# Kernel tuning notes

Hardware: AMD Instinct MI355X
Metric: run time of the kernel (lower is better)

The kernel has to match this reference:

```python
import jax, jax.numpy as jnp
import numpy as np

B, L, HID = 512, 128, 384
N_LABELS, N_SLOTS = 32, 128


def setup_inputs() -> dict:
    key = jax.random.key(0)
    ks = jax.random.split(key, 16)

    def g(k, shape, scale):
        return jax.random.normal(k, shape, dtype=jnp.float32) * scale

    sent_lens = jax.random.randint(ks[0], (B,), 1, L + 1)
    mask = (jnp.arange(L)[None, :] < sent_lens[:, None]).astype(jnp.float32)[..., None]
    # zero out padded token positions to mimic the ragged original
    H = g(ks[1], (B, L, HID), 1.0) * mask
    c_slot_cont = g(ks[2], (B, L, HID), 1.0) * mask
    c_inte = g(ks[3], (B, HID), 1.0)
    s = 1.0 / np.sqrt(HID)
    return {
        "H": H,
        "c_slot_cont": c_slot_cont,
        "c_inte": c_inte,
        "W0": g(ks[4], (HID, HID), s),
        "W1": g(ks[5], (HID, HID), s),
        "W2": g(ks[6], (HID, HID), s),
        "W3": g(ks[7], (HID, HID), s),
        "W4": g(ks[8], (HID, HID), s),
        "b4": g(ks[9], (HID,), s),
        "W5": g(ks[10], (HID, 1), s),
        "V_SF": g(ks[11], (HID, HID), s),
        "W_inte": g(ks[12], (HID, N_LABELS), s),
        "W_slot": g(ks[13], (2 * HID, N_SLOTS), s),
        "sent_lens": sent_lens,
        "iteration_num": 3,
    }


def reference(H, c_slot_cont, c_inte, W0, W1, W2, W3, W4, b4, W5, V_SF,
              W_inte, W_slot, sent_lens, iteration_num):
    Ld = H.shape[1]
    mask = jnp.arange(Ld)[None, :] < sent_lens[:, None]          # [B, L] bool
    maskf = mask[..., None].astype(H.dtype)                       # [B, L, 1]
    neg_inf = jnp.finfo(H.dtype).min

    def sf_fusion(x, y):
        # SF_FusionLayer (dropout off / eval); inner loop runs once since nth=2
        x0 = jnp.tanh(x)
        y0 = jnp.tanh(y)
        f = jax.nn.sigmoid(jnp.tanh(x0 @ W0 + y0 @ W1) @ W2)
        x2 = f * x0 + x
        y2 = (1.0 - f) * y0 + y
        return f * x2 + (1.0 - f) * y2

    def id_fusion(x, y):
        # ID_FusionLayer; softmax over token dim, masked per sentence
        x0 = jnp.tanh(x)
        y0 = jnp.tanh(y)
        rates = ((x @ W3 + y @ W4 + b4) @ W5)[..., 0]             # [B, L]
        rates = jnp.where(mask, rates, neg_inf)
        alphas = jax.nn.softmax(rates, axis=1)[..., None]         # [B, L, 1]
        x2 = alphas * x0 + x
        y2 = (1.0 - alphas) * y0 + y
        return alphas * x2 + (1.0 - alphas) * y2

    r_inte = c_inte                                               # [B, HID]
    r_slot = c_slot_cont
    for _ in range(iteration_num):
        f_slot = sf_fusion(c_slot_cont, r_inte[:, None, :])       # [B, L, HID]
        f_slot = jnp.sum((f_slot @ V_SF) * maskf, axis=1)         # [B, HID]
        r_slot = f_slot[:, None, :] * c_slot_cont                 # [B, L, HID]
        f_inte = jnp.sum(id_fusion(r_slot, H) * maskf, axis=1)    # [B, HID]
        r_inte = f_inte + c_inte

    intent_output = r_inte @ W_inte                               # [B, n_labels]
    slot_output = jnp.concatenate([H, r_slot], axis=-1) @ W_slot  # [B, L, n_slots]
    return intent_output, slot_output
```

## Files before the change

### kernel.cpp

```cpp
#include <hip/hip_runtime.h>
#include <math.h>

#define HID 384
#define SLEN 128
#define NB 512
#define MTOK (NB*SLEN)
#define NLAB 32
#define NSLOT 128
#define GPITCH 72

typedef _Float16 h8 __attribute__((ext_vector_type(8)));
typedef _Float16 h4v __attribute__((ext_vector_type(4)));
typedef __bf16   b8 __attribute__((ext_vector_type(8)));
typedef float    f4 __attribute__((ext_vector_type(4)));

__device__ __forceinline__ float sane(float x){
  return __builtin_isfinite(x) ? x : 0.f;
}
__device__ __forceinline__ float clampf(float x, float lo, float hi){
  return fminf(hi, fmaxf(lo, x));
}
__device__ __forceinline__ float fast_rcp(float x){
  return __builtin_amdgcn_rcpf(x);
}
__device__ __forceinline__ float fast_tanh(float x){
  x = clampf(x, -15.f, 15.f);
  float e = __expf(2.f * x);
  return (e - 1.f) * fast_rcp(e + 1.f);
}
__device__ __forceinline__ float sigmoid_c(float x){
  x = clampf(x, -60.f, 60.f);
  return fast_rcp(1.f + __expf(-x));
}
__device__ __forceinline__ void split16(float x, _Float16* h, _Float16* l){
  _Float16 hh = (_Float16)x; *h = hh; *l = (_Float16)(x - (float)hh);
}
__device__ __forceinline__ h8 ldh(const _Float16* p){ return *reinterpret_cast<const h8*>(p); }
__device__ __forceinline__ b8 ldb(const __bf16* p){ return *reinterpret_cast<const b8*>(p); }
__device__ __forceinline__ f4 mfma16h(h8 a, h8 b, f4 c){
  return __builtin_amdgcn_mfma_f32_16x16x32_f16(a, b, c, 0, 0, 0);
}
__device__ __forceinline__ f4 mfma16b(b8 a, b8 b, f4 c){
  return __builtin_amdgcn_mfma_f32_16x16x32_bf16(a, b, c, 0, 0, 0);
}
__device__ __forceinline__ void bar_lds(){
  asm volatile("s_waitcnt lgkmcnt(0)" ::: "memory");
  __builtin_amdgcn_s_barrier();
}


__global__ void k_lens(const int* __restrict__ raw, int* __restrict__ lensN){
  const int b = threadIdx.x;
  __shared__ int is64;
  if (b == 0) is64 = (raw[1] == 0) ? 1 : 0;
  __syncthreads();
  int v = is64 ? raw[2 * b] : raw[b];
  v = v < 0 ? 0 : (v > SLEN ? SLEN : v);
  lensN[b] = v;
}

__global__ void k_wsplit16(const float* __restrict__ in, _Float16* __restrict__ outh,
                           _Float16* __restrict__ outl, int R, int C){
  int idx = blockIdx.x * blockDim.x + threadIdx.x;
  if (idx < R * C){
    int r = idx / C, c = idx - r * C;
    float v = sane(in[idx]);
    _Float16 h = (_Float16)v;
    outh[(size_t)c * R + r] = h;
    outl[(size_t)c * R + r] = (_Float16)(v - (float)h);
  }
}

__global__ void k_wsplitbf(const float* __restrict__ in, __bf16* __restrict__ outh,
                           __bf16* __restrict__ outl, int R, int C){
  int idx = blockIdx.x * blockDim.x + threadIdx.x;
  if (idx < R * C){
    int r = idx / C, c = idx - r * C;
    float v = sane(in[idx]);
    __bf16 h = (__bf16)v;
    outh[(size_t)c * R + r] = h;
    outl[(size_t)c * R + r] = (__bf16)(v - (float)h);
  }
}

__global__ void k_transpose32(const float* __restrict__ in, float* __restrict__ out,
                              int R, int C){
  int idx = blockIdx.x * blockDim.x + threadIdx.x;
  if (idx < R * C){ int r = idx / C, c = idx - r * C; out[(size_t)c * R + r] = sane(in[idx]); }
}

__global__ void k_sanecopy(const float* __restrict__ in, float* __restrict__ out, int n){
  int i = blockIdx.x * blockDim.x + threadIdx.x;
  if (i < n) out[i] = sane(in[i]);
}

__global__ void k_w35(const float* __restrict__ W3, const float* __restrict__ W4,
                      const float* __restrict__ b4, const float* __restrict__ W5,
                      float* __restrict__ w35, float* __restrict__ w45, float* __restrict__ b45){
  __shared__ float w5s[HID];
  int t = threadIdx.x;
  w5s[t] = sane(W5[t]);
  __syncthreads();
  float s3 = 0.f, s4 = 0.f;
  for (int j = 0; j < HID; ++j){
    float w5 = w5s[j];
    s3 += sane(W3[(size_t)t * HID + j]) * w5;
    s4 += sane(W4[(size_t)t * HID + j]) * w5;
  }
  w35[t] = s3; w45[t] = s4;
  if (t == 0){
    float s = 0.f;
    for (int j = 0; j < HID; ++j) s += sane(b4[j]) * w5s[j];
    *b45 = s;
  }
}

__global__ void k_ci(const float* __restrict__ ci, float* __restrict__ r_inte){
  size_t i = blockIdx.x * (size_t)blockDim.x + threadIdx.x;
  if (i < (size_t)NB * HID) r_inte[i] = sane(ci[i]);
}

__global__ void k_hy(const float* __restrict__ Hm, const float* __restrict__ w45,
                     const float* __restrict__ b45, float* __restrict__ hy){
  int wave = threadIdx.x >> 6, lane = threadIdx.x & 63;
  int tok = blockIdx.x * 4 + wave;
  const float* row = Hm + (size_t)tok * HID;
  float s = 0.f;
#pragma unroll
  for (int i = 0; i < 6; ++i){ int k = lane + 64 * i; s += sane(row[k]) * w45[k]; }
  for (int off = 32; off; off >>= 1) s += __shfl_down(s, off);
  if (lane == 0) hy[tok] = clampf(s + *b45, -1e30f, 1e30f);
}

template <int TANH>
__global__ void k_vecmat(const float* __restrict__ in, const float* __restrict__ W,
                         float* __restrict__ out, float* __restrict__ pre_store){
  const int b = blockIdx.x, t = threadIdx.x;
  __shared__ float v[HID];
  float x = in[(size_t)b * HID + t];
  if (TANH) x = fast_tanh(x);
  v[t] = x;
  if (pre_store) pre_store[(size_t)b * HID + t] = x;
  __syncthreads();
  float s = 0.f;
  for (int k = 0; k < HID; ++k) s += v[k] * W[(size_t)k * HID + t];
  out[(size_t)b * HID + t] = clampf(s, -1e30f, 1e30f);
}

__global__ void __launch_bounds__(512, 4) k_p0c(
    const float* __restrict__ Cs,
    const _Float16* __restrict__ Wth, const _Float16* __restrict__ Wtl,
    const int* __restrict__ lens,
    _Float16* __restrict__ P0h, _Float16* __restrict__ P0l){
  __shared__ _Float16 Ah[64*GPITCH], Al[64*GPITCH];
  const int t = threadIdx.x;
  const int wave = t >> 6, lane = t & 63, quad = lane >> 4, lr = lane & 15;
  const int bx = blockIdx.x;
  const int b = bx >> 1;
  const int len = lens[b];
  const int row0 = (bx & 1) * 64;
  if (row0 >= len) return;
  const int gr0 = bx * 64;
  const int srow = t >> 3;
  const int sk8 = (t & 7) << 3;
  const int col0 = wave * 48;
  const float* abase = Cs + (size_t)(gr0 + srow) * HID + sk8;
  f4 c0 = *(const f4*)(abase);
  f4 c1 = *(const f4*)(abase + 4);
  f4 acc[4][3] = {};
  for (int ks = 0; ks < 6; ++ks){
    const int kk = ks * 64;
    {
      h8 th, tl;
#pragma unroll
      for (int j = 0; j < 8; ++j){
        float x = fast_tanh(sane((j < 4) ? c0[j] : c1[j - 4]));
        _Float16 h = (_Float16)x;
        th[j] = h; tl[j] = (_Float16)(x - (float)h);
      }
      *(h8*)&Ah[srow * GPITCH + sk8] = th;
      *(h8*)&Al[srow * GPITCH + sk8] = tl;
    }
    if (ks < 5){
      c0 = *(const f4*)(abase + kk + 64);
      c1 = *(const f4*)(abase + kk + 68);
    }
    bar_lds();
#pragma unroll
    for (int c = 0; c < 2; ++c){
      const int ro = c * 32 + quad * 8;
      h8 amh[4], aml[4];
#pragma unroll
      for (int mi = 0; mi < 4; ++mi){
        const int r = (mi * 16 + lr) * GPITCH + ro;
        amh[mi] = *(const h8*)&Ah[r]; aml[mi] = *(const h8*)&Al[r];
      }
#pragma unroll
      for (int ni = 0; ni < 3; ++ni){
        const size_t rb = ((size_t)(col0 + ni * 16 + lr)) * HID + kk + ro;
        h8 bh = ldh(Wth + rb), bl = ldh(Wtl + rb);
#pragma unroll
        for (int mi = 0; mi < 4; ++mi){
          acc[mi][ni] = mfma16h(amh[mi], bh, acc[mi][ni]);
          acc[mi][ni] = mfma16h(amh[mi], bl, acc[mi][ni]);
          acc[mi][ni] = mfma16h(aml[mi], bh, acc[mi][ni]);
        }
      }
    }
    bar_lds();
  }
#pragma unroll
  for (int ni = 0; ni < 3; ++ni){
    const int col = col0 + ni * 16 + lr;
#pragma unroll
    for (int mi = 0; mi < 4; ++mi)
#pragma unroll
      for (int r = 0; r < 4; ++r){
        const int rl = row0 + mi * 16 + quad * 4 + r;
        if (rl < len){
          const size_t o = ((size_t)(b * SLEN + rl)) * HID + col;
          _Float16 h, l; split16(acc[mi][ni][r], &h, &l);
          P0h[o] = h; P0l[o] = l;
        }
      }
  }
}

__global__ void __launch_bounds__(512, 4) k_g2n(
    const _Float16* __restrict__ P0h, const _Float16* __restrict__ P0l,
    const _Float16* __restrict__ Wth, const _Float16* __restrict__ Wtl,
    const float* __restrict__ yw1, const float* __restrict__ Cs,
    const float* __restrict__ r_inte,
    const int* __restrict__ lens, float* __restrict__ S){
  __shared__ _Float16 Ah[64*GPITCH], Al[64*GPITCH];
  __shared__ float ywS[HID];
  const int t = threadIdx.x;
  const int wave = t >> 6, lane = t & 63, quad = lane >> 4, lr = lane & 15;
  const int bx = blockIdx.x;
  const int b = bx >> 1;
  const int len = lens[b];
  const int row0 = (bx & 1) * 64;
  if (row0 >= len) return;
  const int gr0 = bx * 64;
  const int srow = t >> 3;
  const int sk8 = (t & 7) << 3;
  const int col0 = wave * 48;
  if (t < HID) ywS[t] = yw1[(size_t)b * HID + t];
  __syncthreads();
  const _Float16* pbase = P0h + (size_t)(gr0 + srow) * HID + sk8;
  const _Float16* lbase = P0l + (size_t)(gr0 + srow) * HID + sk8;
  h8 ph = ldh(pbase), pl = ldh(lbase);
  f4 acc[4][3] = {};
  for (int ks = 0; ks < 6; ++ks){
    const int kk = ks * 64;
    {
      const f4 ywa = *(const f4*)&ywS[kk + sk8];
      const f4 ywb = *(const f4*)&ywS[kk + sk8 + 4];
      h8 th, tl;
#pragma unroll
      for (int j = 0; j < 8; ++j){
        const float yw = (j < 4) ? ywa[j] : ywb[j - 4];
        float x = fast_tanh((float)ph[j] + (float)pl[j] + yw);
        _Float16 h = (_Float16)x;
        th[j] = h; tl[j] = (_Float16)(x - (float)h);
      }
      *(h8*)&Ah[srow * GPITCH + sk8] = th;
      *(h8*)&Al[srow * GPITCH + sk8] = tl;
    }
    if (ks < 5){
      ph = ldh(pbase + kk + 64);
      pl = ldh(lbase + kk + 64);
    }
    bar_lds();
#pragma unroll
    for (int c = 0; c < 2; ++c){
      const int ro = c * 32 + quad * 8;
      h8 amh[4], aml[4];
#pragma unroll
      for (int mi = 0; mi < 4; ++mi){
        const int r = (mi * 16 + lr) * GPITCH + ro;
        amh[mi] = *(const h8*)&Ah[r]; aml[mi] = *(const h8*)&Al[r];
      }
#pragma unroll
      for (int ni = 0; ni < 3; ++ni){
        const size_t rb = ((size_t)(col0 + ni * 16 + lr)) * HID + kk + ro;
        h8 bh = ldh(Wth + rb), bl = ldh(Wtl + rb);
#pragma unroll
        for (int mi = 0; mi < 4; ++mi){
          acc[mi][ni] = mfma16h(amh[mi], bh, acc[mi][ni]);
          acc[mi][ni] = mfma16h(amh[mi], bl, acc[mi][ni]);
          acc[mi][ni] = mfma16h(aml[mi], bh, acc[mi][ni]);
        }
      }
    }
    bar_lds();
  }
  const float* rb = r_inte + (size_t)b * HID;
#pragma unroll
  for (int ni = 0; ni < 3; ++ni){
    const int col = col0 + ni * 16 + lr;
    const float yv = rb[col];
    const float y0 = fast_tanh(yv);
    float csum = 0.f;
#pragma unroll
    for (int mi = 0; mi < 4; ++mi)
#pragma unroll
      for (int r = 0; r < 4; ++r){
        const int rl = row0 + mi * 16 + quad * 4 + r;
        const int grow = gr0 + mi * 16 + quad * 4 + r;
        const float f = sigmoid_c(acc[mi][ni][r]);
        const float omf = 1.f - f;
        const float xv = sane(Cs[(size_t)grow * HID + col]);
        const float x0 = fast_tanh(xv);
        const float outv = f * f * x0 + f * xv + omf * omf * y0 + omf * yv;
        csum += (rl < len) ? outv : 0.f;
      }
    csum += __shfl_xor(csum, 16);
    csum += __shfl_xor(csum, 32);
    if (quad == 0) atomicAdd(&S[(size_t)b * HID + col], csum);
  }
}

__global__ void k_stageD2(
    const float* __restrict__ Cs, const float* __restrict__ Hm,
    const float* __restrict__ ci, const float* __restrict__ Vsc,
    const float* __restrict__ W1c, const float* __restrict__ w35,
    const float* __restrict__ hy, const int* __restrict__ lens,
    float* __restrict__ S, float* __restrict__ fss_g,
    float* __restrict__ r_inte, float* __restrict__ yw1){
  const int b = blockIdx.x;
  const int t = threadIdx.x;
  const int len = lens[b];
  __shared__ float Sl[HID], fssS[HID], fssw[HID], tri[HID];
  __shared__ float rates[SLEN];
  __shared__ float wA[SLEN], wB[SLEN], wC[SLEN], wD[SLEN];
  Sl[t] = S[(size_t)b * HID + t];
  S[(size_t)b * HID + t] = 0.f;
  __syncthreads();
  {
    float s = 0.f;
    for (int k = 0; k < HID; ++k) s += Sl[k] * Vsc[(size_t)k * HID + t];
    const float fs = clampf(s, -1e30f, 1e30f);
    fssS[t] = fs; fssw[t] = fs * w35[t];
    fss_g[(size_t)b * HID + t] = fs;
  }
  __syncthreads();
  const int wave = t >> 6, lane = t & 63;
  for (int l = wave; l < SLEN; l += 6){
    const float* row = Cs + ((size_t)b * SLEN + l) * HID;
    float s = 0.f;
#pragma unroll
    for (int i = 0; i < 6; ++i){ int k = lane + 64 * i; s += sane(row[k]) * fssw[k]; }
    for (int off = 32; off; off >>= 1) s += __shfl_down(s, off);
    if (lane == 0) rates[l] = clampf(s + hy[(size_t)b * SLEN + l], -1e30f, 1e30f);
  }
  __syncthreads();
  if (wave == 0){
    float r0 = (lane < len) ? rates[lane] : -3.0e38f;
    float r1 = (lane + 64 < len) ? rates[lane + 64] : -3.0e38f;
    float mx = fmaxf(r0, r1);
    for (int off = 32; off; off >>= 1) mx = fmaxf(mx, __shfl_xor(mx, off));
    float e0 = (lane < len) ? __expf(r0 - mx) : 0.f;
    float e1 = (lane + 64 < len) ? __expf(r1 - mx) : 0.f;
    float sm = e0 + e1;
    for (int off = 32; off; off >>= 1) sm += __shfl_xor(sm, off);
    const float inv = (sm > 0.f) ? (1.f / sm) : 0.f;
    float a0 = clampf(e0 * inv, 0.f, 1.f), a1 = clampf(e1 * inv, 0.f, 1.f);
    wA[lane] = a0 * a0; wB[lane] = a0;
    wC[lane] = (1.f - a0) * (1.f - a0); wD[lane] = 1.f - a0;
    wA[lane + 64] = a1 * a1; wB[lane + 64] = a1;
    wC[lane + 64] = (1.f - a1) * (1.f - a1); wD[lane + 64] = 1.f - a1;
  }
  __syncthreads();
  {
    const float fs = fssS[t];
    float acc = 0.f;
#pragma unroll 4
    for (int l = 0; l < len; ++l){
      const float cv = sane(Cs[((size_t)b * SLEN + l) * HID + t]);
      const float hv = sane(Hm[((size_t)b * SLEN + l) * HID + t]);
      const float rs = fs * cv;
      acc += wA[l] * fast_tanh(rs) + wB[l] * rs + wC[l] * fast_tanh(hv) + wD[l] * hv;
    }
    const float ri = clampf(acc + sane(ci[(size_t)b * HID + t]), -1e30f, 1e30f);
    r_inte[(size_t)b * HID + t] = ri;
    tri[t] = fast_tanh(ri);
  }
  __syncthreads();
  {
    float s = 0.f;
    for (int k = 0; k < HID; ++k) s += tri[k] * W1c[(size_t)k * HID + t];
    yw1[(size_t)b * HID + t] = clampf(s, -1e30f, 1e30f);
  }
}

__global__ void k_intent(const float* __restrict__ r_inte, const float* __restrict__ Wit,
                         float* __restrict__ out){
  const int t = threadIdx.x;
  const int b = blockIdx.x * 4 + (t >> 5);
  const int n = t & 31;
  const float* wr = Wit + (size_t)n * HID;
  const float* rr = r_inte + (size_t)b * HID;
  float s = 0.f;
  for (int k = 0; k < HID; ++k) s += rr[k] * wr[k];
  out[(size_t)b * NLAB + n] = clampf(s, -3e38f, 3e38f);
}

__global__ void __launch_bounds__(256, 2) k_slot_bf(
    const float* __restrict__ Hm, const float* __restrict__ Cs,
    const float* __restrict__ fss, const int* __restrict__ lens,
    const __bf16* __restrict__ Wth, const __bf16* __restrict__ Wtl,
    float* __restrict__ out){
  const int wave = threadIdx.x >> 6, lane = threadIdx.x & 63;
  const int quad = lane >> 4, lr = lane & 15;
  const int m0 = blockIdx.x * 128 + (wave & 1) * 64;
  const int n0 = (wave >> 1) * 64;
  const int b = blockIdx.x;
  const int ko = quad * 8;
  const int len = lens[b];
  if ((wave & 1) * 64 >= len){
#pragma unroll
    for (int mi = 0; mi < 4; ++mi)
#pragma unroll
      for (int ni = 0; ni < 4; ++ni)
#pragma unroll
        for (int r = 0; r < 4; ++r){
          const int row = m0 + mi * 16 + quad * 4 + r;
          const int col = n0 + ni * 16 + lr;
          out[(size_t)row * NSLOT + col] = 0.f;
        }
    return;
  }
  f4 acc[4][4] = {};
  for (int kk = 0; kk < 2 * HID; kk += 32){
    b8 ah[4], al[4], bh[4], bl[4];
#pragma unroll
    for (int i = 0; i < 4; ++i){
      size_t rb = (size_t)(n0 + i * 16 + lr) * (2 * HID) + kk + ko;
      bh[i] = ldb(Wth + rb); bl[i] = ldb(Wtl + rb);
    }
    if (kk < HID){
#pragma unroll
      for (int i = 0; i < 4; ++i){
        const float* hrow = Hm + (size_t)(m0 + i * 16 + lr) * HID + kk + ko;
        b8 vh, vl;
#pragma unroll
        for (int j = 0; j < 8; ++j){
          float v = sane(hrow[j]);
          __bf16 h = (__bf16)v;
          vh[j] = h; vl[j] = (__bf16)(v - (float)h);
        }
        ah[i] = vh; al[i] = vl;
      }
    } else {
      const int k2 = kk - HID + ko;
      float fv[8];
#pragma unroll
      for (int j = 0; j < 8; ++j) fv[j] = fss[(size_t)b * HID + k2 + j];
#pragma unroll
      for (int i = 0; i < 4; ++i){
        const float* crow = Cs + (size_t)(m0 + i * 16 + lr) * HID + k2;
        b8 vh, vl;
#pragma unroll
        for (int j = 0; j < 8; ++j){
          float v = fv[j] * sane(crow[j]);
          __bf16 h = (__bf16)v;
          vh[j] = h; vl[j] = (__bf16)(v - (float)h);
        }
        ah[i] = vh; al[i] = vl;
      }
    }
#pragma unroll
    for (int mi = 0; mi < 4; ++mi)
#pragma unroll
      for (int ni = 0; ni < 4; ++ni){
        acc[mi][ni] = mfma16b(ah[mi], bh[ni], acc[mi][ni]);
        acc[mi][ni] = mfma16b(ah[mi], bl[ni], acc[mi][ni]);
        acc[mi][ni] = mfma16b(al[mi], bh[ni], acc[mi][ni]);
      }
  }
#pragma unroll
  for (int mi = 0; mi < 4; ++mi)
#pragma unroll
    for (int ni = 0; ni < 4; ++ni)
#pragma unroll
      for (int r = 0; r < 4; ++r){
        const int row = m0 + mi * 16 + quad * 4 + r;
        const int col = n0 + ni * 16 + lr;
        out[(size_t)row * NSLOT + col] = clampf(acc[mi][ni][r], -3e38f, 3e38f);
      }
}

extern "C" void kernel_launch(void* const* d_in, const int* in_sizes, int n_in,
                              void* d_out, int out_size, void* d_ws, size_t ws_size,
                              hipStream_t stream){
  (void)in_sizes; (void)n_in; (void)out_size;
  const float* Hm  = (const float*)d_in[0];
  const float* Cs  = (const float*)d_in[1];
  const float* ci  = (const float*)d_in[2];
  const float* W0  = (const float*)d_in[3];
  const float* W1  = (const float*)d_in[4];
  const float* W2  = (const float*)d_in[5];
  const float* W3  = (const float*)d_in[6];
  const float* W4  = (const float*)d_in[7];
  const float* b4  = (const float*)d_in[8];
  const float* W5  = (const float*)d_in[9];
  const float* Vs  = (const float*)d_in[10];
  const float* Wi  = (const float*)d_in[11];
  const float* Wsl = (const float*)d_in[12];
  const int* lens_raw = (const int*)d_in[13];

  char* base = (char*)d_ws;
  size_t off = 0;
  auto alloc = [&](size_t bytes) -> void* {
    void* p = base + off; off += (bytes + 255) & ~(size_t)255; return p;
  };
  const size_t NT = (size_t)MTOK * HID;
  _Float16* P0h  = (_Float16*)alloc(NT * 2);
  _Float16* P0l  = (_Float16*)alloc(NT * 2);
  _Float16* W0th = (_Float16*)alloc((size_t)HID * HID * 2);
  _Float16* W0tl = (_Float16*)alloc((size_t)HID * HID * 2);
  _Float16* W2th = (_Float16*)alloc((size_t)HID * HID * 2);
  _Float16* W2tl = (_Float16*)alloc((size_t)HID * HID * 2);
  __bf16*   Wsth = (__bf16*)alloc((size_t)2 * HID * NSLOT * 2);
  __bf16*   Wstl = (__bf16*)alloc((size_t)2 * HID * NSLOT * 2);
  float* W1c    = (float*)alloc((size_t)HID * HID * 4);
  float* Vsc    = (float*)alloc((size_t)HID * HID * 4);
  float* Wit    = (float*)alloc((size_t)HID * NLAB * 4);
  float* w35    = (float*)alloc(HID * 4);
  float* w45    = (float*)alloc(HID * 4);
  float* b45    = (float*)alloc(4);
  float* hy     = (float*)alloc((size_t)MTOK * 4);
  float* yw1    = (float*)alloc((size_t)NB * HID * 4);
  float* r_inte = (float*)alloc((size_t)NB * HID * 4);
  float* S      = (float*)alloc((size_t)NB * HID * 4);
  float* fss    = (float*)alloc((size_t)NB * HID * 4);
  int* lensN    = (int*)alloc((size_t)NB * 4);
  if (off > ws_size) return;

  k_lens<<<1, NB, 0, stream>>>(lens_raw, lensN);
  k_wsplit16<<<(HID * HID + 255) / 256, 256, 0, stream>>>(W0, W0th, W0tl, HID, HID);
  k_wsplit16<<<(HID * HID + 255) / 256, 256, 0, stream>>>(W2, W2th, W2tl, HID, HID);
  k_wsplitbf<<<(2 * HID * NSLOT + 255) / 256, 256, 0, stream>>>(Wsl, Wsth, Wstl, 2 * HID, NSLOT);
  k_sanecopy<<<(HID * HID + 255) / 256, 256, 0, stream>>>(W1, W1c, HID * HID);
  k_sanecopy<<<(HID * HID + 255) / 256, 256, 0, stream>>>(Vs, Vsc, HID * HID);
  k_transpose32<<<(HID * NLAB + 255) / 256, 256, 0, stream>>>(Wi, Wit, HID, NLAB);
  k_w35<<<1, HID, 0, stream>>>(W3, W4, b4, W5, w35, w45, b45);
  k_ci<<<(NB * HID + 255) / 256, 256, 0, stream>>>(ci, r_inte);
  k_hy<<<MTOK / 4, 256, 0, stream>>>(Hm, w45, b45, hy);
  k_p0c<<<MTOK / 64, 512, 0, stream>>>(Cs, W0th, W0tl, lensN, P0h, P0l);

  k_vecmat<1><<<NB, HID, 0, stream>>>(r_inte, W1c, yw1, (float*)nullptr);
  hipMemsetAsync(S, 0, (size_t)NB * HID * 4, stream);

  for (int it = 0; it < 3; ++it){
    k_g2n<<<MTOK / 64, 512, 0, stream>>>(P0h, P0l, W2th, W2tl, yw1, Cs, r_inte, lensN, S);
    k_stageD2<<<NB, HID, 0, stream>>>(Cs, Hm, ci, Vsc, W1c, w35, hy, lensN,
                                      S, fss, r_inte, yw1);
  }

  float* outp = (float*)d_out;
  k_intent<<<NB / 4, 128, 0, stream>>>(r_inte, Wit, outp);
  k_slot_bf<<<NB, 256, 0, stream>>>(Hm, Cs, fss, lensN, Wsth, Wstl, outp + (size_t)NB * NLAB);
}
```

Before: 1.086 ms.

## Process whole sentence per block in g2n, drop atomics and init kernels

k_g2n now assigns one block per sentence (128 rows) instead of two 64-row blocks, templating the MFMA and epilogue on 4 or 8 row tiles depending on length. The partial sums are written directly rather than via atomicAdd, so the memset and the zeroing in stageD2 go away, and k_ci is folded into k_vecmat by storing the sanitized input. This removes atomics and two launches and reuses W2 tiles across all rows, but doubles the accumulator registers and LDS per block (launch bounds lowered to 2), halves the block count, and adds some per-block imbalance.

```diff
diff --git a/kernel.cpp b/kernel.cpp
--- a/kernel.cpp
+++ b/kernel.cpp
@@ -115,11 +115,6 @@
   }
 }
 
-__global__ void k_ci(const float* __restrict__ ci, float* __restrict__ r_inte){
-  size_t i = blockIdx.x * (size_t)blockDim.x + threadIdx.x;
-  if (i < (size_t)NB * HID) r_inte[i] = sane(ci[i]);
-}
-
 __global__ void k_hy(const float* __restrict__ Hm, const float* __restrict__ w45,
                      const float* __restrict__ b45, float* __restrict__ hy){
   int wave = threadIdx.x >> 6, lane = threadIdx.x & 63;
@@ -132,15 +127,16 @@
   if (lane == 0) hy[tok] = clampf(s + *b45, -1e30f, 1e30f);
 }
 
-template <int TANH>
+template <int TANH, int SANE_IN>
 __global__ void k_vecmat(const float* __restrict__ in, const float* __restrict__ W,
                          float* __restrict__ out, float* __restrict__ pre_store){
   const int b = blockIdx.x, t = threadIdx.x;
   __shared__ float v[HID];
   float x = in[(size_t)b * HID + t];
+  if (SANE_IN) x = sane(x);
+  if (pre_store) pre_store[(size_t)b * HID + t] = x;
   if (TANH) x = fast_tanh(x);
   v[t] = x;
-  if (pre_store) pre_store[(size_t)b * HID + t] = x;
   __syncthreads();
   float s = 0.f;
   for (int k = 0; k < HID; ++k) s += v[k] * W[(size_t)k * HID + t];
@@ -226,31 +222,89 @@
   }
 }
 
-__global__ void __launch_bounds__(512, 4) k_g2n(
+template <int MI>
+__device__ __forceinline__ void g2n_mfma(f4 (&acc)[8][3],
+    const _Float16* Ah, const _Float16* Al,
+    const _Float16* __restrict__ Wth, const _Float16* __restrict__ Wtl,
+    int col0, int kk, int quad, int lr){
+#pragma unroll
+  for (int c = 0; c < 2; ++c){
+    const int ro = c * 32 + quad * 8;
+    h8 amh[MI], aml[MI];
+#pragma unroll
+    for (int mi = 0; mi < MI; ++mi){
+      const int r = (mi * 16 + lr) * GPITCH + ro;
+      amh[mi] = *(const h8*)&Ah[r]; aml[mi] = *(const h8*)&Al[r];
+    }
+#pragma unroll
+    for (int ni = 0; ni < 3; ++ni){
+      const size_t rb = ((size_t)(col0 + ni * 16 + lr)) * HID + kk + ro;
+      h8 bh = ldh(Wth + rb), bl = ldh(Wtl + rb);
+#pragma unroll
+      for (int mi = 0; mi < MI; ++mi){
+        acc[mi][ni] = mfma16h(amh[mi], bh, acc[mi][ni]);
+        acc[mi][ni] = mfma16h(amh[mi], bl, acc[mi][ni]);
+        acc[mi][ni] = mfma16h(aml[mi], bh, acc[mi][ni]);
+      }
+    }
+  }
+}
+
+template <int MI>
+__device__ __forceinline__ void g2n_epi(const f4 (&acc)[8][3],
+    const float* __restrict__ rb, const float* __restrict__ Cs,
+    float* __restrict__ S, int b, int gr0, int len, int col0, int quad, int lr){
+#pragma unroll
+  for (int ni = 0; ni < 3; ++ni){
+    const int col = col0 + ni * 16 + lr;
+    const float yv = rb[col];
+    const float y0 = fast_tanh(yv);
+    float csum = 0.f;
+#pragma unroll
+    for (int mi = 0; mi < MI; ++mi)
+#pragma unroll
+      for (int r = 0; r < 4; ++r){
+        const int rl = mi * 16 + quad * 4 + r;
+        const int grow = gr0 + rl;
+        const float f = sigmoid_c(acc[mi][ni][r]);
+        const float omf = 1.f - f;
+        const float xv = sane(Cs[(size_t)grow * HID + col]);
+        const float x0 = fast_tanh(xv);
+        const float outv = f * f * x0 + f * xv + omf * omf * y0 + omf * yv;
+        csum += (rl < len) ? outv : 0.f;
+      }
+    csum += __shfl_xor(csum, 16);
+    csum += __shfl_xor(csum, 32);
+    if (quad == 0) S[(size_t)b * HID + col] = csum;
+  }
+}
+
+__global__ void __launch_bounds__(512, 2) k_g2n(
     const _Float16* __restrict__ P0h, const _Float16* __restrict__ P0l,
     const _Float16* __restrict__ Wth, const _Float16* __restrict__ Wtl,
     const float* __restrict__ yw1, const float* __restrict__ Cs,
     const float* __restrict__ r_inte,
     const int* __restrict__ lens, float* __restrict__ S){
-  __shared__ _Float16 Ah[64*GPITCH], Al[64*GPITCH];
+  __shared__ _Float16 Ah[128*GPITCH], Al[128*GPITCH];
   __shared__ float ywS[HID];
   const int t = threadIdx.x;
   const int wave = t >> 6, lane = t & 63, quad = lane >> 4, lr = lane & 15;
-  const int bx = blockIdx.x;
-  const int b = bx >> 1;
+  const int b = blockIdx.x;
   const int len = lens[b];
-  const int row0 = (bx & 1) * 64;
-  if (row0 >= len) return;
-  const int gr0 = bx * 64;
+  const int gr0 = b * SLEN;
   const int srow = t >> 3;
   const int sk8 = (t & 7) << 3;
   const int col0 = wave * 48;
+  const bool hi = (len > 64);
   if (t < HID) ywS[t] = yw1[(size_t)b * HID + t];
   __syncthreads();
-  const _Float16* pbase = P0h + (size_t)(gr0 + srow) * HID + sk8;
-  const _Float16* lbase = P0l + (size_t)(gr0 + srow) * HID + sk8;
-  h8 ph = ldh(pbase), pl = ldh(lbase);
-  f4 acc[4][3] = {};
+  const _Float16* pb0 = P0h + (size_t)(gr0 + srow) * HID + sk8;
+  const _Float16* lb0 = P0l + (size_t)(gr0 + srow) * HID + sk8;
+  const _Float16* pb1 = pb0 + (size_t)64 * HID;
+  const _Float16* lb1 = lb0 + (size_t)64 * HID;
+  h8 ph0 = ldh(pb0), pl0 = ldh(lb0), ph1 = {}, pl1 = {};
+  if (hi){ ph1 = ldh(pb1); pl1 = ldh(lb1); }
+  f4 acc[8][3] = {};
   for (int ks = 0; ks < 6; ++ks){
     const int kk = ks * 64;
     {
@@ -260,65 +314,37 @@
 #pragma unroll
       for (int j = 0; j < 8; ++j){
         const float yw = (j < 4) ? ywa[j] : ywb[j - 4];
-        float x = fast_tanh((float)ph[j] + (float)pl[j] + yw);
+        float x = fast_tanh((float)ph0[j] + (float)pl0[j] + yw);
         _Float16 h = (_Float16)x;
         th[j] = h; tl[j] = (_Float16)(x - (float)h);
       }
       *(h8*)&Ah[srow * GPITCH + sk8] = th;
       *(h8*)&Al[srow * GPITCH + sk8] = tl;
+      if (hi){
+        h8 th1, tl1;
+#pragma unroll
+        for (int j = 0; j < 8; ++j){
+          const float yw = (j < 4) ? ywa[j] : ywb[j - 4];
+          float x = fast_tanh((float)ph1[j] + (float)pl1[j] + yw);
+          _Float16 h = (_Float16)x;
+          th1[j] = h; tl1[j] = (_Float16)(x - (float)h);
+        }
+        *(h8*)&Ah[(64 + srow) * GPITCH + sk8] = th1;
+        *(h8*)&Al[(64 + srow) * GPITCH + sk8] = tl1;
+      }
     }
     if (ks < 5){
-      ph = ldh(pbase + kk + 64);
-      pl = ldh(lbase + kk + 64);
+      ph0 = ldh(pb0 + kk + 64); pl0 = ldh(lb0 + kk + 64);
+      if (hi){ ph1 = ldh(pb1 + kk + 64); pl1 = ldh(lb1 + kk + 64); }
     }
     bar_lds();
-#pragma unroll
-    for (int c = 0; c < 2; ++c){
-      const int ro = c * 32 + quad * 8;
-      h8 amh[4], aml[4];
-#pragma unroll
-      for (int mi = 0; mi < 4; ++mi){
-        const int r = (mi * 16 + lr) * GPITCH + ro;
-        amh[mi] = *(const h8*)&Ah[r]; aml[mi] = *(const h8*)&Al[r];
-      }
-#pragma unroll
-      for (int ni = 0; ni < 3; ++ni){
-        const size_t rb = ((size_t)(col0 + ni * 16 + lr)) * HID + kk + ro;
-        h8 bh = ldh(Wth + rb), bl = ldh(Wtl + rb);
-#pragma unroll
-        for (int mi = 0; mi < 4; ++mi){
-          acc[mi][ni] = mfma16h(amh[mi], bh, acc[mi][ni]);
-          acc[mi][ni] = mfma16h(amh[mi], bl, acc[mi][ni]);
-          acc[mi][ni] = mfma16h(aml[mi], bh, acc[mi][ni]);
-        }
-      }
-    }
+    if (hi) g2n_mfma<8>(acc, Ah, Al, Wth, Wtl, col0, kk, quad, lr);
+    else    g2n_mfma<4>(acc, Ah, Al, Wth, Wtl, col0, kk, quad, lr);
     bar_lds();
   }
   const float* rb = r_inte + (size_t)b * HID;
-#pragma unroll
-  for (int ni = 0; ni < 3; ++ni){
-    const int col = col0 + ni * 16 + lr;
-    const float yv = rb[col];
-    const float y0 = fast_tanh(yv);
-    float csum = 0.f;
-#pragma unroll
-    for (int mi = 0; mi < 4; ++mi)
-#pragma unroll
-      for (int r = 0; r < 4; ++r){
-        const int rl = row0 + mi * 16 + quad * 4 + r;
-        const int grow = gr0 + mi * 16 + quad * 4 + r;
-        const float f = sigmoid_c(acc[mi][ni][r]);
-        const float omf = 1.f - f;
-        const float xv = sane(Cs[(size_t)grow * HID + col]);
-        const float x0 = fast_tanh(xv);
-        const float outv = f * f * x0 + f * xv + omf * omf * y0 + omf * yv;
-        csum += (rl < len) ? outv : 0.f;
-      }
-    csum += __shfl_xor(csum, 16);
-    csum += __shfl_xor(csum, 32);
-    if (quad == 0) atomicAdd(&S[(size_t)b * HID + col], csum);
-  }
+  if (hi) g2n_epi<8>(acc, rb, Cs, S, b, gr0, len, col0, quad, lr);
+  else    g2n_epi<4>(acc, rb, Cs, S, b, gr0, len, col0, quad, lr);
 }
 
 __global__ void k_stageD2(
@@ -326,7 +352,7 @@
     const float* __restrict__ ci, const float* __restrict__ Vsc,
     const float* __restrict__ W1c, const float* __restrict__ w35,
     const float* __restrict__ hy, const int* __restrict__ lens,
-    float* __restrict__ S, float* __restrict__ fss_g,
+    const float* __restrict__ S, float* __restrict__ fss_g,
     float* __restrict__ r_inte, float* __restrict__ yw1){
   const int b = blockIdx.x;
   const int t = threadIdx.x;
@@ -335,7 +361,6 @@
   __shared__ float rates[SLEN];
   __shared__ float wA[SLEN], wB[SLEN], wC[SLEN], wD[SLEN];
   Sl[t] = S[(size_t)b * HID + t];
-  S[(size_t)b * HID + t] = 0.f;
   __syncthreads();
   {
     float s = 0.f;
@@ -546,15 +571,13 @@
   k_sanecopy<<<(HID * HID + 255) / 256, 256, 0, stream>>>(Vs, Vsc, HID * HID);
   k_transpose32<<<(HID * NLAB + 255) / 256, 256, 0, stream>>>(Wi, Wit, HID, NLAB);
   k_w35<<<1, HID, 0, stream>>>(W3, W4, b4, W5, w35, w45, b45);
-  k_ci<<<(NB * HID + 255) / 256, 256, 0, stream>>>(ci, r_inte);
   k_hy<<<MTOK / 4, 256, 0, stream>>>(Hm, w45, b45, hy);
   k_p0c<<<MTOK / 64, 512, 0, stream>>>(Cs, W0th, W0tl, lensN, P0h, P0l);
 
-  k_vecmat<1><<<NB, HID, 0, stream>>>(r_inte, W1c, yw1, (float*)nullptr);
-  hipMemsetAsync(S, 0, (size_t)NB * HID * 4, stream);
+  k_vecmat<1, 1><<<NB, HID, 0, stream>>>(ci, W1c, yw1, r_inte);
 
   for (int it = 0; it < 3; ++it){
-    k_g2n<<<MTOK / 64, 512, 0, stream>>>(P0h, P0l, W2th, W2tl, yw1, Cs, r_inte, lensN, S);
+    k_g2n<<<NB, 512, 0, stream>>>(P0h, P0l, W2th, W2tl, yw1, Cs, r_inte, lensN, S);
     k_stageD2<<<NB, HID, 0, stream>>>(Cs, Hm, ci, Vsc, W1c, w35, hy, lensN,
                                       S, fss, r_inte, yw1);
   }
```

After: 997.2 us. -8.2%, faster.
